# Kernel tuning notes

Hardware: AMD Instinct MI355X
Metric: run time of the kernel (lower is better)

## Reference

```python
import jax, jax.numpy as jnp
import numpy as np

N = 50000
P = 200000
L = 6
IN_DIM = 128
OUT_DIM = 128
HEADS = 4


def setup_inputs() -> dict:
    key = jax.random.key(0)
    ks = jax.random.split(key, 7)
    x = jax.random.normal(ks[0], (N, IN_DIM), dtype=jnp.float32)
    path_list = jax.random.randint(ks[1], (P, L), 0, N, dtype=jnp.int64)
    s = 0.1
    w_ih = jax.random.normal(ks[2], (3 * OUT_DIM, IN_DIM), dtype=jnp.float32) * s
    w_hh = jax.random.normal(ks[3], (3 * OUT_DIM, OUT_DIM), dtype=jnp.float32) * s
    b_ih = jax.random.normal(ks[4], (3 * OUT_DIM,), dtype=jnp.float32) * s
    b_hh = jax.random.normal(ks[5], (3 * OUT_DIM,), dtype=jnp.float32) * s
    a = jax.random.uniform(ks[6], (OUT_DIM, HEADS), dtype=jnp.float32) * 2.0 - 1.0
    return {"x": x, "path_list": path_list, "w_ih": w_ih, "w_hh": w_hh,
            "b_ih": b_ih, "b_hh": b_hh, "a": a}


def _gru_final_hidden(feats, w_ih, w_hh, b_ih, b_hh):
    # feats: [P, L, in_dim]; PyTorch GRU cell semantics, h0 = 0.
    out_dim = w_hh.shape[1]
    p = feats.shape[0]

    def step(h, xt):
        gi = xt @ w_ih.T + b_ih          # [P, 3*out]
        gh = h @ w_hh.T + b_hh           # [P, 3*out]
        ir, iz, i_n = jnp.split(gi, 3, axis=-1)
        hr, hz, h_n = jnp.split(gh, 3, axis=-1)
        r = jax.nn.sigmoid(ir + hr)
        z = jax.nn.sigmoid(iz + hz)
        n_cand = jnp.tanh(i_n + r * h_n)
        h_new = (1.0 - z) * n_cand + z * h
        return h_new, None

    h0 = jnp.zeros((p, out_dim), feats.dtype)
    xs = jnp.swapaxes(feats, 0, 1)       # [L, P, in_dim]
    h, _ = jax.lax.scan(step, h0, xs)
    return h                              # [P, out_dim]


def reference(x, path_list, w_ih, w_hh, b_ih, b_hh, a):
    n, out_dim = x.shape[0], w_hh.shape[1]
    heads = a.shape[1]
    # F.embedding(path_list, x): gather path features [P, L, in_dim]
    feats = x[path_list]
    path_emb = _gru_final_hidden(feats, w_ih, w_hh, b_ih, b_hh)       # [P, out]
    # unnormalized attention per head
    att_un = jnp.exp(jax.nn.leaky_relu(path_emb @ a, negative_slope=0.2))  # [P, H]
    row = path_list[:, -1]                                             # owner node of each path
    # M @ att_un : segment-sum over owner nodes
    att_sum = jax.ops.segment_sum(att_un, row, num_segments=n)         # [N, H]
    # M.t() @ (1/att_sum) : gather back to paths
    att_low = (1.0 / att_sum)[row]                                     # [P, H]
    att_n = att_un * att_low                                           # [P, H]
    # reshape(-1,1).repeat(1,out).reshape(P,-1): each head's scalar repeated out_dim times
    att_rep = jnp.repeat(att_n, out_dim, axis=1)                       # [P, H*out]
    emb_rep = jnp.tile(path_emb, (1, heads))                           # [P, H*out]
    path_att_emb = att_rep * emb_rep
    node_att_emb = jax.ops.segment_sum(path_att_emb, row, num_segments=n)  # [N, H*out]
    return node_att_emb
```

## Files before the change

### kernel.cpp

```cpp
#include <hip/hip_runtime.h>
#include <hip/hip_bf16.h>
#include <math.h>

#define NN 50000
#define PP 200000
#define LL 6
#define DD 128
#define HH 4

#define TM 64
#define NT 512
#define HPAD 132

typedef __attribute__((ext_vector_type(8))) short short8;
typedef __attribute__((ext_vector_type(4))) float f32x4;

__device__ __forceinline__ unsigned short f2bf(float v) {
    __hip_bfloat16 h = __float2bfloat16(v);
    return *(unsigned short*)&h;
}
__device__ __forceinline__ float fast_rcp(float x) { return __builtin_amdgcn_rcpf(x); }
__device__ __forceinline__ float fast_sigmoid(float x) {
    return fast_rcp(1.f + __expf(-x));
}
__device__ __forceinline__ float fast_tanh(float x) {
    float e = __expf(-2.f * fabsf(x));
    float t = (1.f - e) * fast_rcp(1.f + e);
    return copysignf(t, x);
}

__global__ void prep_x_kernel(const float* __restrict__ x,
                              unsigned short* __restrict__ xb) {
    int i = blockIdx.x * 256 + threadIdx.x;
    if (i < NN * DD) xb[i] = f2bf(x[i]);
}
__global__ void prep_w_kernel(const float* __restrict__ w_ih,
                              const float* __restrict__ w_hh,
                              unsigned short* __restrict__ wib,
                              unsigned short* __restrict__ whb) {
    int i = blockIdx.x * 256 + threadIdx.x;
    if (i < 3 * DD * DD) { wib[i] = f2bf(w_ih[i]); whb[i] = f2bf(w_hh[i]); }
}

__global__ __launch_bounds__(NT, 2)
void gru_att_kernel(const unsigned short* __restrict__ xb,
                    const int*   __restrict__ path_list,
                    const unsigned short* __restrict__ wib,
                    const unsigned short* __restrict__ whb,
                    const float* __restrict__ b_ih,
                    const float* __restrict__ b_hh,
                    const float* __restrict__ a,
                    float* __restrict__ att_sum,
                    float* __restrict__ out)
{
    __shared__ __align__(16) unsigned short hsb[TM * DD];
    __shared__ __align__(16) unsigned short xs [TM * DD];
    __shared__ int   nodes_s[TM * LL];
    __shared__ float hs_f[TM * HPAD];
    __shared__ float attun[TM * HH];
    float* red_s = (float*)xs;

    const int tid  = threadIdx.x;
    const int lane = tid & 63;
    const int wave = tid >> 6;
    const int lcol = lane & 15;
    const int quad = lane >> 4;
    const int d    = wave * 16 + lcol;
    const int p0   = blockIdx.x * TM;
    const int ko   = quad * 8;

    short8 Bx[3][4], Bh[3][4];
    #pragma unroll
    for (int c = 0; c < 3; ++c)
        #pragma unroll
        for (int ks = 0; ks < 4; ++ks) {
            Bx[c][ks] = *(const short8*)(wib + (size_t)(c * DD + d) * DD + ks * 32 + ko);
            Bh[c][ks] = *(const short8*)(whb + (size_t)(c * DD + d) * DD + ks * 32 + ko);
        }
    const float brz = b_ih[d]       + b_hh[d];
    const float bzz = b_ih[d + 128] + b_hh[d + 128];
    const float bin = b_ih[d + 256];
    const float bhn = b_hh[d + 256];

    for (int i = tid; i < TM * LL; i += NT) nodes_s[i] = path_list[(size_t)p0 * LL + i];
    for (int i = tid; i < TM * DD / 8; i += NT)
        ((uint4*)hsb)[i] = make_uint4(0u, 0u, 0u, 0u);

    float hreg[16];
    #pragma unroll
    for (int i = 0; i < 16; ++i) hreg[i] = 0.f;

    __syncthreads();

    const int gpi = tid >> 3;
    const int gtt = tid & 7;
    const int gpm = gpi & 15;

    uint4 xg0, xg1;
    {
        int node = nodes_s[gpi * LL + 0];
        const uint4* src = (const uint4*)(xb + (size_t)node * DD + gtt * 16);
        xg0 = src[0]; xg1 = src[1];
    }

    f32x4 accR[4], accZ[4], accN[4], accH[4];

    #pragma unroll
    for (int t = 0; t < LL; ++t) {
        {
            int kb0 = 2 * gtt, kb1 = 2 * gtt + 1;
            *(uint4*)(xs + gpi * DD + ((kb0 ^ gpm) * 8)) = xg0;
            *(uint4*)(xs + gpi * DD + ((kb1 ^ gpm) * 8)) = xg1;
        }
        __syncthreads();

        if (t < LL - 1) {
            int node = nodes_s[gpi * LL + t + 1];
            const uint4* src = (const uint4*)(xb + (size_t)node * DD + gtt * 16);
            xg0 = src[0]; xg1 = src[1];
        }

        #pragma unroll
        for (int rt = 0; rt < 4; ++rt) {
            accR[rt] = (f32x4){brz, brz, brz, brz};
            accZ[rt] = (f32x4){bzz, bzz, bzz, bzz};
            accN[rt] = (f32x4){bin, bin, bin, bin};
            accH[rt] = (f32x4){bhn, bhn, bhn, bhn};
        }

        #pragma unroll
        for (int ks = 0; ks < 4; ++ks) {
            const int kb = ks * 4 + quad;
            #pragma unroll
            for (int rt = 0; rt < 4; ++rt) {
                const int p = rt * 16 + lcol;
                short8 ax = *(const short8*)(xs  + p * DD + ((kb ^ lcol) * 8));
                short8 ah = *(const short8*)(hsb + p * DD + ((kb ^ lcol) * 8));
                accR[rt] = __builtin_amdgcn_mfma_f32_16x16x32_bf16(ax, Bx[0][ks], accR[rt], 0, 0, 0);
                accZ[rt] = __builtin_amdgcn_mfma_f32_16x16x32_bf16(ax, Bx[1][ks], accZ[rt], 0, 0, 0);
                accN[rt] = __builtin_amdgcn_mfma_f32_16x16x32_bf16(ax, Bx[2][ks], accN[rt], 0, 0, 0);
                accR[rt] = __builtin_amdgcn_mfma_f32_16x16x32_bf16(ah, Bh[0][ks], accR[rt], 0, 0, 0);
                accZ[rt] = __builtin_amdgcn_mfma_f32_16x16x32_bf16(ah, Bh[1][ks], accZ[rt], 0, 0, 0);
                accH[rt] = __builtin_amdgcn_mfma_f32_16x16x32_bf16(ah, Bh[2][ks], accH[rt], 0, 0, 0);
            }
        }
        __syncthreads();

        #pragma unroll
        for (int rt = 0; rt < 4; ++rt) {
            #pragma unroll
            for (int r = 0; r < 4; ++r) {
                const int idx = rt * 4 + r;
                const int p   = rt * 16 + quad * 4 + r;
                float rg = fast_sigmoid(accR[rt][r]);
                float zg = fast_sigmoid(accZ[rt][r]);
                float ng = fast_tanh(accN[rt][r] + rg * accH[rt][r]);
                float hnew = fmaf(zg, hreg[idx] - ng, ng);
                hreg[idx] = hnew;
                if (t < LL - 1) {
                    hsb[p * DD + (((d >> 3) ^ (p & 15)) * 8) + (d & 7)] = f2bf(hnew);
                } else {
                    hs_f[p * HPAD + d] = hnew;
                }
            }
        }
    }

    __syncthreads();

    {
        int pi = tid >> 3, tt = tid & 7;
        float s0 = 0.f, s1 = 0.f, s2 = 0.f, s3 = 0.f;
        #pragma unroll
        for (int j = 0; j < 16; ++j) {
            int dd2 = tt * 16 + j;
            float hv = hs_f[pi * HPAD + dd2];
            float4 av = *(const float4*)(a + dd2 * 4);
            s0 += hv * av.x; s1 += hv * av.y; s2 += hv * av.z; s3 += hv * av.w;
        }
        float* rp = red_s + (pi * 8 + tt) * 4;
        rp[0] = s0; rp[1] = s1; rp[2] = s2; rp[3] = s3;
    }
    __syncthreads();
    if (tid < TM) {
        int pi = tid;
        int row = nodes_s[pi * LL + (LL - 1)];
        #pragma unroll
        for (int h = 0; h < HH; ++h) {
            float s = 0.f;
            #pragma unroll
            for (int tt = 0; tt < 8; ++tt) s += red_s[(pi * 8 + tt) * 4 + h];
            float lv = (s > 0.f) ? s : 0.2f * s;
            float e  = __expf(lv);
            attun[pi * HH + h] = e;
            atomicAdd(&att_sum[row * HH + h], e);
        }
    }
    __syncthreads();

    for (int e = tid; e < TM * 512; e += NT) {
        int pi  = e >> 9;
        int c   = e & 511;
        int h   = c >> 7;
        int dd2 = c & 127;
        int row = nodes_s[pi * LL + (LL - 1)];
        float v = attun[pi * HH + h] * hs_f[pi * HPAD + dd2];
        atomicAdd(&out[(size_t)row * 512 + c], v);
    }
}

__global__ void normalize_kernel(float* __restrict__ out,
                                 const float* __restrict__ att_sum) {
    int i = blockIdx.x * 256 + threadIdx.x;
    if (i < NN * 512) {
        int n = i >> 9;
        int h = (i >> 7) & 3;
        float s = att_sum[n * HH + h];
        float v = out[i];
        out[i] = (s > 0.f) ? v / s : 0.f;
    }
}

extern "C" void kernel_launch(void* const* d_in, const int* in_sizes, int n_in,
                              void* d_out, int out_size, void* d_ws, size_t ws_size,
                              hipStream_t stream) {
    const float* x         = (const float*)d_in[0];
    const int*   path_list = (const int*)  d_in[1];
    const float* w_ih      = (const float*)d_in[2];
    const float* w_hh      = (const float*)d_in[3];
    const float* b_ih      = (const float*)d_in[4];
    const float* b_hh      = (const float*)d_in[5];
    const float* a         = (const float*)d_in[6];
    float* out = (float*)d_out;

    float*          att_sum = (float*)d_ws;
    unsigned short* xb      = (unsigned short*)((char*)d_ws + 800000);
    unsigned short* wib     = xb + (size_t)NN * DD;
    unsigned short* whb     = wib + 3 * DD * DD;

    hipMemsetAsync(out, 0, (size_t)NN * 512 * sizeof(float), stream);
    hipMemsetAsync(att_sum, 0, (size_t)NN * HH * sizeof(float), stream);

    prep_x_kernel<<<(NN * DD + 255) / 256, 256, 0, stream>>>(x, xb);
    prep_w_kernel<<<(3 * DD * DD + 255) / 256, 256, 0, stream>>>(w_ih, w_hh, wib, whb);

    gru_att_kernel<<<PP / TM, NT, 0, stream>>>(xb, path_list, wib, whb,
                                               b_ih, b_hh, a, att_sum, out);

    normalize_kernel<<<(NN * 512 + 255) / 256, 256, 0, stream>>>(out, att_sum);
}
```

Baseline: 725.5 us.

## Replace per-element atomic scatter with sorted-by-owner gather aggregation

```diff
diff --git a/kernel.cpp b/kernel.cpp
--- a/kernel.cpp
+++ b/kernel.cpp
@@ -18,6 +18,9 @@
 __device__ __forceinline__ unsigned short f2bf(float v) {
     __hip_bfloat16 h = __float2bfloat16(v);
     return *(unsigned short*)&h;
+}
+__device__ __forceinline__ float bf2f(unsigned short u) {
+    union { unsigned int i; float f; } c; c.i = ((unsigned int)u) << 16; return c.f;
 }
 __device__ __forceinline__ float fast_rcp(float x) { return __builtin_amdgcn_rcpf(x); }
 __device__ __forceinline__ float fast_sigmoid(float x) {
@@ -40,6 +43,48 @@
                               unsigned short* __restrict__ whb) {
     int i = blockIdx.x * 256 + threadIdx.x;
     if (i < 3 * DD * DD) { wib[i] = f2bf(w_ih[i]); whb[i] = f2bf(w_hh[i]); }
+}
+
+__global__ void histo_kernel(const int* __restrict__ path_list,
+                             int* __restrict__ cnt) {
+    int p = blockIdx.x * 256 + threadIdx.x;
+    if (p < PP) atomicAdd(&cnt[path_list[p * LL + (LL - 1)]], 1);
+}
+
+__global__ void scan_kernel(const int* __restrict__ cnt,
+                            int* __restrict__ offs,
+                            int* __restrict__ cursor) {
+    __shared__ int ls[256];
+    const int t = threadIdx.x;
+    const int chunk = (NN + 255) / 256;
+    int s = 0;
+    for (int j = 0; j < chunk; ++j) {
+        int i = t + j * 256;
+        if (i < NN) s += cnt[i];
+    }
+    ls[t] = s; __syncthreads();
+    for (int off = 1; off < 256; off <<= 1) {
+        int v = (t >= off) ? ls[t - off] : 0;
+        __syncthreads();
+        ls[t] += v;
+        __syncthreads();
+    }
+    int run = (t == 0) ? 0 : ls[t - 1];
+    for (int j = 0; j < chunk; ++j) {
+        int i = t + j * 256;
+        if (i < NN) { offs[i] = run; cursor[i] = run; run += cnt[i]; }
+    }
+}
+
+__global__ void scatter_kernel(const int* __restrict__ path_list,
+                               int* __restrict__ cursor,
+                               int* __restrict__ sorted) {
+    int p = blockIdx.x * 256 + threadIdx.x;
+    if (p < PP) {
+        int row = path_list[p * LL + (LL - 1)];
+        int k = atomicAdd(&cursor[row], 1);
+        sorted[k] = p;
+    }
 }
 
 __global__ __launch_bounds__(NT, 2)
@@ -51,14 +96,15 @@
                     const float* __restrict__ b_hh,
                     const float* __restrict__ a,
                     float* __restrict__ att_sum,
-                    float* __restrict__ out)
+                    unsigned short* __restrict__ emb,
+                    float* __restrict__ att_un_g)
 {
-    __shared__ __align__(16) unsigned short hsb[TM * DD];
-    __shared__ __align__(16) unsigned short xs [TM * DD];
-    __shared__ int   nodes_s[TM * LL];
-    __shared__ float hs_f[TM * HPAD];
-    __shared__ float attun[TM * HH];
-    float* red_s = (float*)xs;
+    __shared__ __align__(16) unsigned char smem[43520];
+    unsigned short* hsb    = (unsigned short*)smem;
+    unsigned short* xs     = (unsigned short*)(smem + 16384);
+    float*          hs_f   = (float*)smem;
+    float*          red_s  = (float*)(smem + 33792);
+    int*            nodes_s= (int*)(smem + 41984);
 
     const int tid  = threadIdx.x;
     const int lane = tid & 63;
@@ -171,13 +217,18 @@
     {
         int pi = tid >> 3, tt = tid & 7;
         float s0 = 0.f, s1 = 0.f, s2 = 0.f, s3 = 0.f;
+        unsigned short pack[16];
         #pragma unroll
         for (int j = 0; j < 16; ++j) {
             int dd2 = tt * 16 + j;
             float hv = hs_f[pi * HPAD + dd2];
+            pack[j] = f2bf(hv);
             float4 av = *(const float4*)(a + dd2 * 4);
             s0 += hv * av.x; s1 += hv * av.y; s2 += hv * av.z; s3 += hv * av.w;
         }
+        uint4* dst = (uint4*)(emb + (size_t)(p0 + pi) * DD + tt * 16);
+        dst[0] = *(uint4*)&pack[0];
+        dst[1] = *(uint4*)&pack[8];
         float* rp = red_s + (pi * 8 + tt) * 4;
         rp[0] = s0; rp[1] = s1; rp[2] = s2; rp[3] = s3;
     }
@@ -185,6 +236,7 @@
     if (tid < TM) {
         int pi = tid;
         int row = nodes_s[pi * LL + (LL - 1)];
+        float4 e4;
         #pragma unroll
         for (int h = 0; h < HH; ++h) {
             float s = 0.f;
@@ -192,33 +244,43 @@
             for (int tt = 0; tt < 8; ++tt) s += red_s[(pi * 8 + tt) * 4 + h];
             float lv = (s > 0.f) ? s : 0.2f * s;
             float e  = __expf(lv);
-            attun[pi * HH + h] = e;
+            ((float*)&e4)[h] = e;
             atomicAdd(&att_sum[row * HH + h], e);
         }
-    }
-    __syncthreads();
-
-    for (int e = tid; e < TM * 512; e += NT) {
-        int pi  = e >> 9;
-        int c   = e & 511;
-        int h   = c >> 7;
-        int dd2 = c & 127;
-        int row = nodes_s[pi * LL + (LL - 1)];
-        float v = attun[pi * HH + h] * hs_f[pi * HPAD + dd2];
-        atomicAdd(&out[(size_t)row * 512 + c], v);
-    }
-}
-
-__global__ void normalize_kernel(float* __restrict__ out,
-                                 const float* __restrict__ att_sum) {
-    int i = blockIdx.x * 256 + threadIdx.x;
-    if (i < NN * 512) {
-        int n = i >> 9;
-        int h = (i >> 7) & 3;
-        float s = att_sum[n * HH + h];
-        float v = out[i];
-        out[i] = (s > 0.f) ? v / s : 0.f;
-    }
+        *(float4*)(att_un_g + (size_t)(p0 + pi) * HH) = e4;
+    }
+}
+
+__global__ __launch_bounds__(256)
+void agg_kernel(const unsigned short* __restrict__ emb,
+                const float* __restrict__ att_un,
+                const float* __restrict__ att_sum,
+                const int* __restrict__ offs,
+                const int* __restrict__ cnt,
+                const int* __restrict__ sorted,
+                float* __restrict__ out)
+{
+    int node = blockIdx.x * 2 + (threadIdx.x >> 7);
+    int d    = threadIdx.x & 127;
+    if (node >= NN) return;
+    int start = offs[node];
+    int len   = cnt[node];
+    float a0 = 0.f, a1 = 0.f, a2 = 0.f, a3 = 0.f;
+    for (int i = 0; i < len; ++i) {
+        int p = sorted[start + i];
+        float4 at = *(const float4*)(att_un + (size_t)p * 4);
+        float ev = bf2f(emb[(size_t)p * DD + d]);
+        a0 = fmaf(at.x, ev, a0);
+        a1 = fmaf(at.y, ev, a1);
+        a2 = fmaf(at.z, ev, a2);
+        a3 = fmaf(at.w, ev, a3);
+    }
+    float4 s = *(const float4*)(att_sum + (size_t)node * 4);
+    float* o = out + (size_t)node * 512 + d;
+    o[0]   = (s.x > 0.f) ? a0 / s.x : 0.f;
+    o[128] = (s.y > 0.f) ? a1 / s.y : 0.f;
+    o[256] = (s.z > 0.f) ? a2 / s.z : 0.f;
+    o[384] = (s.w > 0.f) ? a3 / s.w : 0.f;
 }
 
 extern "C" void kernel_launch(void* const* d_in, const int* in_sizes, int n_in,
@@ -233,19 +295,31 @@
     const float* a         = (const float*)d_in[6];
     float* out = (float*)d_out;
 
-    float*          att_sum = (float*)d_ws;
-    unsigned short* xb      = (unsigned short*)((char*)d_ws + 800000);
-    unsigned short* wib     = xb + (size_t)NN * DD;
-    unsigned short* whb     = wib + 3 * DD * DD;
-
-    hipMemsetAsync(out, 0, (size_t)NN * 512 * sizeof(float), stream);
-    hipMemsetAsync(att_sum, 0, (size_t)NN * HH * sizeof(float), stream);
+    char* w = (char*)d_ws;
+    float*          att_sum = (float*)w;                 w += 800000;
+    int*            cnt     = (int*)w;                   w += 200000;
+    int*            offs    = (int*)w;                   w += 200000;
+    int*            cursor  = (int*)w;                   w += 200000;
+    int*            sorted  = (int*)w;                   w += 800000;
+    float*          att_un  = (float*)w;                 w += 3200000;
+    unsigned short* xb      = (unsigned short*)w;        w += 12800000;
+    unsigned short* wib     = (unsigned short*)w;        w += 98304;
+    unsigned short* whb     = (unsigned short*)w;        w += 98304;
+    unsigned short* emb     = (unsigned short*)w;        w += 51200000;
+
+    hipMemsetAsync(att_sum, 0, 800000, stream);
+    hipMemsetAsync(cnt, 0, 200000, stream);
 
     prep_x_kernel<<<(NN * DD + 255) / 256, 256, 0, stream>>>(x, xb);
     prep_w_kernel<<<(3 * DD * DD + 255) / 256, 256, 0, stream>>>(w_ih, w_hh, wib, whb);
 
+    histo_kernel<<<(PP + 255) / 256, 256, 0, stream>>>(path_list, cnt);
+    scan_kernel<<<1, 256, 0, stream>>>(cnt, offs, cursor);
+    scatter_kernel<<<(PP + 255) / 256, 256, 0, stream>>>(path_list, cursor, sorted);
+
     gru_att_kernel<<<PP / TM, NT, 0, stream>>>(xb, path_list, wib, whb,
-                                               b_ih, b_hh, a, att_sum, out);
-
-    normalize_kernel<<<(NN * 512 + 255) / 256, 256, 0, stream>>>(out, att_sum);
-}
+                                               b_ih, b_hh, a, att_sum, emb, att_un);
+
+    agg_kernel<<<(NN + 1) / 2, 256, 0, stream>>>(emb, att_un, att_sum,
+                                                 offs, cnt, sorted, out);
+}
```

Result: faster. 654.9 us (-9.7%).
